# Kernel optimization log

Measured on AMD Instinct MI355X. Metric: run time of the kernel, lower is better.

Reference implementation:

```python
import jax, jax.numpy as jnp
import numpy as np

RATIO = 0.5  # SAGPooling ratio


def setup_inputs() -> dict:
    key = jax.random.key(0)
    ks = jax.random.split(key, 6)
    B, n, d, out_dim, Eg = 128, 512, 256, 256, 4096  # graphs, nodes/graph, feat, proj out, edges/graph
    N = B * n
    x = jax.random.normal(ks[0], (N, d), dtype=jnp.float32)
    # edges connect nodes within the same graph (contiguous node blocks)
    src = jax.random.randint(ks[1], (B, Eg), 0, n)
    dst = jax.random.randint(ks[2], (B, Eg), 0, n)
    off = (jnp.arange(B) * n)[:, None]
    edge_index = jnp.stack([(src + off).reshape(-1), (dst + off).reshape(-1)]).astype(jnp.int32)
    batch = jnp.repeat(jnp.arange(B), n).astype(jnp.int32)
    s = 1.0 / np.sqrt(d).astype(np.float32)
    w_rel = jax.random.normal(ks[3], (d, 1), dtype=jnp.float32) * s   # GraphConv lin_rel (has bias)
    b_rel = jnp.zeros((1,), dtype=jnp.float32)
    w_root = jax.random.normal(ks[4], (d, 1), dtype=jnp.float32) * s  # GraphConv lin_root (no bias)
    w_proj = jax.random.normal(ks[5], (d, out_dim), dtype=jnp.float32) * s  # projection Linear
    b_proj = jnp.zeros((out_dim,), dtype=jnp.float32)
    return {"x": x, "edge_index": edge_index, "batch": batch, "num_graphs": B,
            "w_rel": w_rel, "b_rel": b_rel, "w_root": w_root,
            "w_proj": w_proj, "b_proj": b_proj}


def reference(x, edge_index, batch, num_graphs, w_rel, b_rel, w_root, w_proj, b_proj):
    N, d = x.shape
    n = N // num_graphs                    # equal-size graphs
    k = int(np.ceil(RATIO * n))            # PyG topk: ceil(ratio * num_nodes)
    src, dst = edge_index[0], edge_index[1]
    # GraphConv(node_dim, 1): score_i = lin_rel(sum_{j->i} x_j) + lin_root(x_i)
    agg = jax.ops.segment_sum(x[src], dst, num_segments=N)          # [N, d]
    score = jnp.tanh((agg @ w_rel + b_rel + x @ w_root)[:, 0])       # [N], tanh nonlinearity
    sb = score.reshape(num_graphs, n)                                # [B, n]
    top_vals, top_idx = jax.lax.top_k(sb, k)                         # per-graph topk
    xb = x.reshape(num_graphs, n, d)
    x_sel = jnp.take_along_axis(xb, top_idx[:, :, None], axis=1)     # [B, k, d]
    x_sel = x_sel * top_vals[:, :, None]                             # x[perm] * score[perm] (multiplier=1)
    pooled = x_sel.mean(axis=1)                                      # global_mean_pool over k kept nodes
    return pooled @ w_proj + b_proj                                  # [B, out_dim]
```

## Files before the change

### kernel.cpp

```cpp
#include <hip/hip_runtime.h>

#define D        256
#define NPG      512
#define BG       128
#define KSEL     256
#define EPG      4096
#define NN       (BG * NPG)
#define ET       (BG * EPG)

__global__ __launch_bounds__(256) void k_proj_scores(
        const float* __restrict__ x,
        const float* __restrict__ w_rel, const float* __restrict__ w_root,
        float* __restrict__ p, float* __restrict__ r) {
    int tid  = threadIdx.x;
    int wave = tid >> 6, lane = tid & 63;
    int node = blockIdx.x * 4 + wave;

    const float4* x4  = (const float4*)(x + (size_t)node * D);
    const float4* wr4 = (const float4*)w_rel;
    const float4* wo4 = (const float4*)w_root;
    float4 xv = x4[lane];
    float4 wr = wr4[lane];
    float4 wo = wo4[lane];
    float pv = xv.x * wr.x + xv.y * wr.y + xv.z * wr.z + xv.w * wr.w;
    float rv = xv.x * wo.x + xv.y * wo.y + xv.z * wo.z + xv.w * wo.w;
    #pragma unroll
    for (int off = 32; off; off >>= 1) {
        pv += __shfl_xor(pv, off, 64);
        rv += __shfl_xor(rv, off, 64);
    }
    if (lane == 0) { p[node] = pv; r[node] = rv; }
}

__global__ __launch_bounds__(1024) void k_fused(
        const float* __restrict__ x, const int* __restrict__ ei,
        const float* __restrict__ p, const float* __restrict__ r,
        const float* __restrict__ b_rel,
        const float* __restrict__ w_proj, const float* __restrict__ b_proj,
        float* __restrict__ out) {
    __shared__ float s_p[NPG];
    __shared__ float s_r[NPG];
    __shared__ float s_agg[NPG];
    __shared__ float s_val[NPG];
    __shared__ int   s_cnt2[1024];
    __shared__ int   s_selid[KSEL];
    __shared__ float s_selv[KSEL];
    __shared__ float s_pool[D];
    __shared__ float s_red[4][D];
    __shared__ int   s_nsel;

    int b = blockIdx.x, tid = threadIdx.x;
    int base = b * NPG;

    if (tid < NPG) { s_p[tid] = p[base + tid]; s_agg[tid] = 0.f; }
    else           { int j = tid - NPG; s_r[j] = r[base + j]; }
    if (tid < D)   s_pool[tid] = 0.f;
    if (tid == 0)  s_nsel = 0;
    __syncthreads();

    const int* src = ei + (size_t)b * EPG;
    const int* dst = ei + ET + (size_t)b * EPG;
    #pragma unroll
    for (int e = tid; e < EPG; e += 1024)
        atomicAdd(&s_agg[dst[e] - base], s_p[src[e] - base]);
    __syncthreads();

    float brel = b_rel[0];
    if (tid < NPG)
        s_val[tid] = tanhf(s_agg[tid] + brel + s_r[tid]);
    __syncthreads();

    {
        int j = tid & (NPG - 1);
        int half = tid >> 9;
        float sv = s_val[j];
        int lo = half * 256;
        int c = 0;
        #pragma unroll 8
        for (int i = lo; i < lo + 256; ++i) {
            float o = s_val[i];
            c += (o > sv) || (o == sv && i < j);
        }
        s_cnt2[tid] = c;
    }
    __syncthreads();
    if (tid < NPG) {
        int rank = s_cnt2[tid] + s_cnt2[tid + NPG];
        if (rank < KSEL) {
            int pos = atomicAdd(&s_nsel, 1);
            s_selid[pos] = tid;
            s_selv[pos]  = s_val[tid];
        }
    }
    __syncthreads();

    {
        int wave = tid >> 6, lane = tid & 63;
        float4 acc = {0.f, 0.f, 0.f, 0.f};
        #pragma unroll 4
        for (int m = 0; m < 16; ++m) {
            int s   = wave * 16 + m;
            int row = s_selid[s];
            float v = s_selv[s];
            float4 xv = ((const float4*)(x + (size_t)(base + row) * D))[lane];
            acc.x += v * xv.x; acc.y += v * xv.y;
            acc.z += v * xv.z; acc.w += v * xv.w;
        }
        atomicAdd(&s_pool[lane * 4 + 0], acc.x);
        atomicAdd(&s_pool[lane * 4 + 1], acc.y);
        atomicAdd(&s_pool[lane * 4 + 2], acc.z);
        atomicAdd(&s_pool[lane * 4 + 3], acc.w);
    }
    __syncthreads();

    {
        int f = tid & (D - 1);
        int q = tid >> 8;
        float partial = 0.f;
        int k0 = q * 64;
        #pragma unroll 8
        for (int kk = k0; kk < k0 + 64; ++kk)
            partial += s_pool[kk] * w_proj[kk * D + f];
        s_red[q][f] = partial;
    }
    __syncthreads();
    if (tid < D)
        out[(size_t)b * D + tid] = b_proj[tid] +
            (s_red[0][tid] + s_red[1][tid] + s_red[2][tid] + s_red[3][tid]) * (1.0f / KSEL);
}

extern "C" void kernel_launch(void* const* d_in, const int* in_sizes, int n_in,
                              void* d_out, int out_size, void* d_ws, size_t ws_size,
                              hipStream_t stream) {
    const float* x      = (const float*)d_in[0];
    const int*   ei     = (const int*)d_in[1];
    const float* w_rel  = (const float*)d_in[4];
    const float* b_rel  = (const float*)d_in[5];
    const float* w_root = (const float*)d_in[6];
    const float* w_proj = (const float*)d_in[7];
    const float* b_proj = (const float*)d_in[8];
    float* out = (float*)d_out;

    float* p = (float*)d_ws;
    float* r = p + NN;

    k_proj_scores<<<NN / 4, 256, 0, stream>>>(x, w_rel, w_root, p, r);
    k_fused<<<BG, 1024, 0, stream>>>(x, ei, p, r, b_rel, w_proj, b_proj, out);
}
```

Measured before the change: 136.2 us.

## Split fused select/pool/project kernel into three kernels for more parallelism

The single per-graph fused kernel becomes three kernels. Selection runs one block per graph and writes the chosen indices and scores to workspace. Pooling splits each graph across 4 blocks of 512 threads, and a separate projection kernel sums the partials and applies w_proj. The aim is to put more blocks on the gather-heavy pooling phase, which previously ran on only 128 blocks, and to drop the shared-memory atomics. In exchange it adds two kernel launches and round-trips through global memory.

```diff
diff --git a/kernel.cpp b/kernel.cpp
--- a/kernel.cpp
+++ b/kernel.cpp
@@ -17,11 +17,9 @@
     int node = blockIdx.x * 4 + wave;
 
     const float4* x4  = (const float4*)(x + (size_t)node * D);
-    const float4* wr4 = (const float4*)w_rel;
-    const float4* wo4 = (const float4*)w_root;
     float4 xv = x4[lane];
-    float4 wr = wr4[lane];
-    float4 wo = wo4[lane];
+    float4 wr = ((const float4*)w_rel)[lane];
+    float4 wo = ((const float4*)w_root)[lane];
     float pv = xv.x * wr.x + xv.y * wr.y + xv.z * wr.z + xv.w * wr.w;
     float rv = xv.x * wo.x + xv.y * wo.y + xv.z * wo.z + xv.w * wo.w;
     #pragma unroll
@@ -32,29 +30,21 @@
     if (lane == 0) { p[node] = pv; r[node] = rv; }
 }
 
-__global__ __launch_bounds__(1024) void k_fused(
-        const float* __restrict__ x, const int* __restrict__ ei,
+__global__ __launch_bounds__(1024) void k_select(
+        const int* __restrict__ ei,
         const float* __restrict__ p, const float* __restrict__ r,
         const float* __restrict__ b_rel,
-        const float* __restrict__ w_proj, const float* __restrict__ b_proj,
-        float* __restrict__ out) {
+        int* __restrict__ selid, float* __restrict__ selv) {
     __shared__ float s_p[NPG];
-    __shared__ float s_r[NPG];
     __shared__ float s_agg[NPG];
     __shared__ float s_val[NPG];
     __shared__ int   s_cnt2[1024];
-    __shared__ int   s_selid[KSEL];
-    __shared__ float s_selv[KSEL];
-    __shared__ float s_pool[D];
-    __shared__ float s_red[4][D];
     __shared__ int   s_nsel;
 
     int b = blockIdx.x, tid = threadIdx.x;
     int base = b * NPG;
 
     if (tid < NPG) { s_p[tid] = p[base + tid]; s_agg[tid] = 0.f; }
-    else           { int j = tid - NPG; s_r[j] = r[base + j]; }
-    if (tid < D)   s_pool[tid] = 0.f;
     if (tid == 0)  s_nsel = 0;
     __syncthreads();
 
@@ -67,7 +57,7 @@
 
     float brel = b_rel[0];
     if (tid < NPG)
-        s_val[tid] = tanhf(s_agg[tid] + brel + s_r[tid]);
+        s_val[tid] = tanhf(s_agg[tid] + brel + r[base + tid]);
     __syncthreads();
 
     {
@@ -88,45 +78,58 @@
         int rank = s_cnt2[tid] + s_cnt2[tid + NPG];
         if (rank < KSEL) {
             int pos = atomicAdd(&s_nsel, 1);
-            s_selid[pos] = tid;
-            s_selv[pos]  = s_val[tid];
+            selid[b * KSEL + pos] = tid;
+            selv [b * KSEL + pos] = s_val[tid];
         }
     }
+}
+
+__global__ __launch_bounds__(512) void k_pool(
+        const float* __restrict__ x,
+        const int* __restrict__ selid, const float* __restrict__ selv,
+        float* __restrict__ ppool) {
+    __shared__ float s_red[8][D];
+    int blk = blockIdx.x;
+    int b = blk >> 2, part = blk & 3;
+    int tid = threadIdx.x, wave = tid >> 6, lane = tid & 63;
+    int base = b * NPG;
+    const int*   sid = selid + b * KSEL + part * 64;
+    const float* sv  = selv  + b * KSEL + part * 64;
+
+    float4 acc = {0.f, 0.f, 0.f, 0.f};
+    #pragma unroll
+    for (int m = 0; m < 8; ++m) {
+        int s   = wave * 8 + m;
+        int row = sid[s];
+        float v = sv[s];
+        float4 xv = ((const float4*)(x + (size_t)(base + row) * D))[lane];
+        acc.x += v * xv.x; acc.y += v * xv.y;
+        acc.z += v * xv.z; acc.w += v * xv.w;
+    }
+    ((float4*)s_red[wave])[lane] = acc;
     __syncthreads();
+    if (tid < D) {
+        float s = 0.f;
+        #pragma unroll
+        for (int w = 0; w < 8; ++w) s += s_red[w][tid];
+        ppool[(size_t)blk * D + tid] = s;
+    }
+}
 
-    {
-        int wave = tid >> 6, lane = tid & 63;
-        float4 acc = {0.f, 0.f, 0.f, 0.f};
-        #pragma unroll 4
-        for (int m = 0; m < 16; ++m) {
-            int s   = wave * 16 + m;
-            int row = s_selid[s];
-            float v = s_selv[s];
-            float4 xv = ((const float4*)(x + (size_t)(base + row) * D))[lane];
-            acc.x += v * xv.x; acc.y += v * xv.y;
-            acc.z += v * xv.z; acc.w += v * xv.w;
-        }
-        atomicAdd(&s_pool[lane * 4 + 0], acc.x);
-        atomicAdd(&s_pool[lane * 4 + 1], acc.y);
-        atomicAdd(&s_pool[lane * 4 + 2], acc.z);
-        atomicAdd(&s_pool[lane * 4 + 3], acc.w);
-    }
+__global__ __launch_bounds__(256) void k_project(
+        const float* __restrict__ ppool,
+        const float* __restrict__ w_proj, const float* __restrict__ b_proj,
+        float* __restrict__ out) {
+    __shared__ float s_pool[D];
+    int b = blockIdx.x, tid = threadIdx.x;
+    const float* pp = ppool + (size_t)b * 4 * D;
+    s_pool[tid] = pp[tid] + pp[D + tid] + pp[2 * D + tid] + pp[3 * D + tid];
     __syncthreads();
-
-    {
-        int f = tid & (D - 1);
-        int q = tid >> 8;
-        float partial = 0.f;
-        int k0 = q * 64;
-        #pragma unroll 8
-        for (int kk = k0; kk < k0 + 64; ++kk)
-            partial += s_pool[kk] * w_proj[kk * D + f];
-        s_red[q][f] = partial;
-    }
-    __syncthreads();
-    if (tid < D)
-        out[(size_t)b * D + tid] = b_proj[tid] +
-            (s_red[0][tid] + s_red[1][tid] + s_red[2][tid] + s_red[3][tid]) * (1.0f / KSEL);
+    float acc = 0.f;
+    #pragma unroll 8
+    for (int kk = 0; kk < D; ++kk)
+        acc += s_pool[kk] * w_proj[kk * D + tid];
+    out[(size_t)b * D + tid] = b_proj[tid] + acc * (1.0f / KSEL);
 }
 
 extern "C" void kernel_launch(void* const* d_in, const int* in_sizes, int n_in,
@@ -141,9 +144,14 @@
     const float* b_proj = (const float*)d_in[8];
     float* out = (float*)d_out;
 
-    float* p = (float*)d_ws;
-    float* r = p + NN;
+    float* p     = (float*)d_ws;
+    float* r     = p + NN;
+    int*   selid = (int*)(r + NN);
+    float* selv  = (float*)(selid + BG * KSEL);
+    float* ppool = selv + BG * KSEL;
 
     k_proj_scores<<<NN / 4, 256, 0, stream>>>(x, w_rel, w_root, p, r);
-    k_fused<<<BG, 1024, 0, stream>>>(x, ei, p, r, b_rel, w_proj, b_proj, out);
+    k_select<<<BG, 1024, 0, stream>>>(ei, p, r, b_rel, selid, selv);
+    k_pool<<<BG * 4, 512, 0, stream>>>(x, selid, selv, ppool);
+    k_project<<<BG, 256, 0, stream>>>(ppool, w_proj, b_proj, out);
 }
```

Result: slower. 142.8 us (+4.8%).

## Fuse per-node score projection into per-graph kernel and vectorize LDS loops

Applied to the files above, without the earlier changes.

Removes the separate score-projection kernel and computes the rel/root dot products inside the per-graph block, writing them straight to shared memory instead of global workspace. Also vectorizes the rank-counting loop and the projection matvec with float4 LDS reads, and replaces shared-memory atomics in pooling with a per-wave buffer reduction. This saves a launch and a global round trip, but it concentrates the full read of x on only 128 blocks, which may underuse the GPU's bandwidth.

```diff
diff --git a/kernel.cpp b/kernel.cpp
--- a/kernel.cpp
+++ b/kernel.cpp
@@ -8,78 +8,88 @@
 #define NN       (BG * NPG)
 #define ET       (BG * EPG)
 
-__global__ __launch_bounds__(256) void k_proj_scores(
-        const float* __restrict__ x,
-        const float* __restrict__ w_rel, const float* __restrict__ w_root,
-        float* __restrict__ p, float* __restrict__ r) {
-    int tid  = threadIdx.x;
-    int wave = tid >> 6, lane = tid & 63;
-    int node = blockIdx.x * 4 + wave;
-
-    const float4* x4  = (const float4*)(x + (size_t)node * D);
-    const float4* wr4 = (const float4*)w_rel;
-    const float4* wo4 = (const float4*)w_root;
-    float4 xv = x4[lane];
-    float4 wr = wr4[lane];
-    float4 wo = wo4[lane];
-    float pv = xv.x * wr.x + xv.y * wr.y + xv.z * wr.z + xv.w * wr.w;
-    float rv = xv.x * wo.x + xv.y * wo.y + xv.z * wo.z + xv.w * wo.w;
-    #pragma unroll
-    for (int off = 32; off; off >>= 1) {
-        pv += __shfl_xor(pv, off, 64);
-        rv += __shfl_xor(rv, off, 64);
-    }
-    if (lane == 0) { p[node] = pv; r[node] = rv; }
-}
-
-__global__ __launch_bounds__(1024) void k_fused(
+__global__ __launch_bounds__(1024) void k_mega(
         const float* __restrict__ x, const int* __restrict__ ei,
-        const float* __restrict__ p, const float* __restrict__ r,
-        const float* __restrict__ b_rel,
+        const float* __restrict__ w_rel, const float* __restrict__ b_rel,
+        const float* __restrict__ w_root,
         const float* __restrict__ w_proj, const float* __restrict__ b_proj,
         float* __restrict__ out) {
-    __shared__ float s_p[NPG];
-    __shared__ float s_r[NPG];
-    __shared__ float s_agg[NPG];
-    __shared__ float s_val[NPG];
+    __shared__ __align__(16) float s_p[NPG];
+    __shared__ __align__(16) float s_r[NPG];
+    __shared__ __align__(16) float s_agg[NPG];
+    __shared__ __align__(16) float s_val[NPG];
     __shared__ int   s_cnt2[1024];
     __shared__ int   s_selid[KSEL];
-    __shared__ float s_selv[KSEL];
-    __shared__ float s_pool[D];
-    __shared__ float s_red[4][D];
+    __shared__ __align__(16) float s_selv[KSEL];
+    __shared__ __align__(16) float s_pool[D];
+    __shared__ __align__(16) float s_red[16][D];
     __shared__ int   s_nsel;
 
     int b = blockIdx.x, tid = threadIdx.x;
+    int wave = tid >> 6, lane = tid & 63;
     int base = b * NPG;
 
-    if (tid < NPG) { s_p[tid] = p[base + tid]; s_agg[tid] = 0.f; }
-    else           { int j = tid - NPG; s_r[j] = r[base + j]; }
-    if (tid < D)   s_pool[tid] = 0.f;
+    if (tid < NPG) s_agg[tid] = 0.f;
     if (tid == 0)  s_nsel = 0;
+
+    {
+        int sub = tid & 15;
+        int nid = tid >> 4;
+        float4 wr[4], wo[4];
+        #pragma unroll
+        for (int i = 0; i < 4; ++i) {
+            wr[i] = ((const float4*)w_rel)[i * 16 + sub];
+            wo[i] = ((const float4*)w_root)[i * 16 + sub];
+        }
+        #pragma unroll
+        for (int pass = 0; pass < 8; ++pass) {
+            int node = pass * 64 + nid;
+            const float4* xr = (const float4*)(x + (size_t)(base + node) * D);
+            float pv = 0.f, rv = 0.f;
+            #pragma unroll
+            for (int i = 0; i < 4; ++i) {
+                float4 xv = xr[i * 16 + sub];
+                pv += xv.x * wr[i].x + xv.y * wr[i].y + xv.z * wr[i].z + xv.w * wr[i].w;
+                rv += xv.x * wo[i].x + xv.y * wo[i].y + xv.z * wo[i].z + xv.w * wo[i].w;
+            }
+            #pragma unroll
+            for (int off = 8; off; off >>= 1) {
+                pv += __shfl_xor(pv, off, 64);
+                rv += __shfl_xor(rv, off, 64);
+            }
+            if (sub == 0) { s_p[node] = pv; s_r[node] = rv; }
+        }
+    }
     __syncthreads();
 
-    const int* src = ei + (size_t)b * EPG;
-    const int* dst = ei + ET + (size_t)b * EPG;
-    #pragma unroll
-    for (int e = tid; e < EPG; e += 1024)
-        atomicAdd(&s_agg[dst[e] - base], s_p[src[e] - base]);
+    {
+        const int* src = ei + (size_t)b * EPG;
+        const int* dst = ei + ET + (size_t)b * EPG;
+        #pragma unroll
+        for (int e = tid; e < EPG; e += 1024)
+            atomicAdd(&s_agg[dst[e] - base], s_p[src[e] - base]);
+    }
     __syncthreads();
 
-    float brel = b_rel[0];
     if (tid < NPG)
-        s_val[tid] = tanhf(s_agg[tid] + brel + s_r[tid]);
+        s_val[tid] = tanhf(s_agg[tid] + b_rel[0] + s_r[tid]);
     __syncthreads();
 
     {
         int j = tid & (NPG - 1);
         int half = tid >> 9;
         float sv = s_val[j];
-        int lo = half * 256;
+        int lo = half * (NPG / 2);
+        const float4* v4 = (const float4*)(s_val + lo);
         int c = 0;
         #pragma unroll 8
-        for (int i = lo; i < lo + 256; ++i) {
-            float o = s_val[i];
-            c += (o > sv) || (o == sv && i < j);
+        for (int q = 0; q < NPG / 8; ++q) {
+            float4 o = v4[q];
+            int i0 = lo + q * 4;
+            c += (o.x > sv) || (o.x == sv && (i0 + 0) < j);
+            c += (o.y > sv) || (o.y == sv && (i0 + 1) < j);
+            c += (o.z > sv) || (o.z == sv && (i0 + 2) < j);
+            c += (o.w > sv) || (o.w == sv && (i0 + 3) < j);
         }
         s_cnt2[tid] = c;
     }
@@ -95,9 +105,8 @@
     __syncthreads();
 
     {
-        int wave = tid >> 6, lane = tid & 63;
         float4 acc = {0.f, 0.f, 0.f, 0.f};
-        #pragma unroll 4
+        #pragma unroll
         for (int m = 0; m < 16; ++m) {
             int s   = wave * 16 + m;
             int row = s_selid[s];
@@ -106,22 +115,32 @@
             acc.x += v * xv.x; acc.y += v * xv.y;
             acc.z += v * xv.z; acc.w += v * xv.w;
         }
-        atomicAdd(&s_pool[lane * 4 + 0], acc.x);
-        atomicAdd(&s_pool[lane * 4 + 1], acc.y);
-        atomicAdd(&s_pool[lane * 4 + 2], acc.z);
-        atomicAdd(&s_pool[lane * 4 + 3], acc.w);
+        ((float4*)s_red[wave])[lane] = acc;
+    }
+    __syncthreads();
+    if (tid < D) {
+        float s = 0.f;
+        #pragma unroll
+        for (int w = 0; w < 16; ++w) s += s_red[w][tid];
+        s_pool[tid] = s;
     }
     __syncthreads();
 
     {
         int f = tid & (D - 1);
         int q = tid >> 8;
-        float partial = 0.f;
-        int k0 = q * 64;
-        #pragma unroll 8
-        for (int kk = k0; kk < k0 + 64; ++kk)
-            partial += s_pool[kk] * w_proj[kk * D + f];
-        s_red[q][f] = partial;
+        const float4* pool4 = (const float4*)s_pool + q * 16;
+        const float* wp = w_proj + (size_t)(q * 64) * D + f;
+        float acc = 0.f;
+        #pragma unroll
+        for (int t = 0; t < 16; ++t) {
+            float4 pv = pool4[t];
+            acc += pv.x * wp[(t * 4 + 0) * D];
+            acc += pv.y * wp[(t * 4 + 1) * D];
+            acc += pv.z * wp[(t * 4 + 2) * D];
+            acc += pv.w * wp[(t * 4 + 3) * D];
+        }
+        s_red[q][f] = acc;
     }
     __syncthreads();
     if (tid < D)
@@ -141,9 +160,5 @@
     const float* b_proj = (const float*)d_in[8];
     float* out = (float*)d_out;
 
-    float* p = (float*)d_ws;
-    float* r = p + NN;
-
-    k_proj_scores<<<NN / 4, 256, 0, stream>>>(x, w_rel, w_root, p, r);
-    k_fused<<<BG, 1024, 0, stream>>>(x, ei, p, r, b_rel, w_proj, b_proj, out);
+    k_mega<<<BG, 1024, 0, stream>>>(x, ei, w_rel, b_rel, w_root, w_proj, b_proj, out);
 }
```

New measurement: 135.7 us. No clear change (-0.3%).
